# Optimization experiments

Measured on AMD Instinct MI355X. Metric: run time of the kernel, lower is better.

The kernel has to match this reference:

```python
import jax, jax.numpy as jnp
import numpy as np

N, E, F_IN, HID, OUT, H = 50000, 500000, 128, 64, 64, 2
P_DROP = 0.2


def setup_inputs() -> dict:
    key = jax.random.key(0)
    ks = jax.random.split(key, 24)
    g = lambda k, shp: jax.random.normal(k, shp, jnp.float32) * 0.05
    inp = {
        "feat": jax.random.normal(ks[0], (N, F_IN), jnp.float32),
        "edge_src": jax.random.randint(ks[1], (E,), 0, N, jnp.int32),
        "edge_dst": jax.random.randint(ks[2], (E,), 0, N, jnp.int32),
        # feature-mask linears
        "Wmt": g(ks[3], (F_IN, F_IN)), "bmt": g(ks[4], (F_IN,)),
        "Wms": g(ks[5], (F_IN, F_IN)), "bms": g(ks[6], (F_IN,)),
        # SAGEConv layers (mean aggregator): self + neigh linear + bias
        "W1_self": g(ks[7], (F_IN, HID)), "W1_neigh": g(ks[8], (F_IN, HID)), "b1": g(ks[9], (HID,)),
        "W2_self": g(ks[10], (HID, OUT)), "W2_neigh": g(ks[11], (HID, OUT)), "b2": g(ks[12], (OUT,)),
        # GATv2Conv layers: fc_src, fc_dst, attn vector per head, bias
        "g1_Wsrc": g(ks[13], (F_IN, H * HID)), "g1_Wdst": g(ks[14], (F_IN, H * HID)),
        "g1_attn": g(ks[15], (H, HID)), "g1_bias": g(ks[16], (H * HID,)),
        "g2_Wsrc": g(ks[17], (HID, H * OUT)), "g2_Wdst": g(ks[18], (HID, H * OUT)),
        "g2_attn": g(ks[19], (H, OUT)), "g2_bias": g(ks[20], (H * OUT,)),
        # final projection
        "W3": g(ks[21], (OUT + F_IN, OUT)), "b3": g(ks[22], (OUT,)),
    }
    # deterministic (inverted) dropout masks, training=True, p=0.2
    keep = 1.0 - P_DROP
    km1, km2 = jax.random.split(ks[23])
    inp["drop_t"] = jax.random.bernoulli(km1, keep, (N, HID)).astype(jnp.float32) / keep
    inp["drop_s"] = jax.random.bernoulli(km2, keep, (N, HID)).astype(jnp.float32) / keep
    return inp


def _sage_mean(h, src, dst, W_self, W_neigh, b):
    # mean over in-neighbors, then linear (mean and linear commute)
    agg = jax.ops.segment_sum(h[src], dst, num_segments=N)          # [N,D]
    deg = jax.ops.segment_sum(jnp.ones((E,), h.dtype), dst, num_segments=N)
    h_neigh = agg / jnp.maximum(deg, 1.0)[:, None]
    return h @ W_self + h_neigh @ W_neigh + b


def _gatv2(h, src, dst, Wsrc, Wdst, attn, bias, heads, dout):
    fs = (h @ Wsrc).reshape(N, heads, dout)
    fd = (h @ Wdst).reshape(N, heads, dout)
    e = jax.nn.leaky_relu(fs[src] + fd[dst], 0.2)                   # [E,H,D]
    logits = jnp.einsum('ehd,hd->eh', e, attn)                      # [E,H]
    m = jax.ops.segment_max(logits, dst, num_segments=N)            # edge softmax per dst
    ex = jnp.exp(logits - m[dst])
    denom = jax.ops.segment_sum(ex, dst, num_segments=N)
    alpha = ex / denom[dst]                                         # [E,H]
    out = jax.ops.segment_sum(alpha[:, :, None] * fs[src], dst, num_segments=N)
    return out + bias.reshape(heads, dout)                          # [N,H,D]


def _l2norm(x):
    return x / jnp.maximum(jnp.linalg.norm(x, axis=1, keepdims=True), 1e-12)


def reference(feat, edge_src, edge_dst, Wmt, bmt, Wms, bms,
              W1_self, W1_neigh, b1, W2_self, W2_neigh, b2,
              g1_Wsrc, g1_Wdst, g1_attn, g1_bias,
              g2_Wsrc, g2_Wdst, g2_attn, g2_bias,
              W3, b3, drop_t, drop_s):
    gelu = lambda x: jax.nn.gelu(x, approximate=False)  # torch F.gelu default = exact erf
    # topology branch (SAGE)
    h_t = feat * jax.nn.sigmoid(feat @ Wmt + bmt)
    h_t = gelu(_sage_mean(h_t, edge_src, edge_dst, W1_self, W1_neigh, b1)) * drop_t
    h_t = gelu(_sage_mean(h_t, edge_src, edge_dst, W2_self, W2_neigh, b2))
    h_t = jnp.concatenate([h_t, feat], axis=1) @ W3 + b3
    h_t = _l2norm(jax.nn.leaky_relu(h_t, 0.01))
    # semantic branch (GATv2)
    h_s = feat * jax.nn.sigmoid(feat @ Wms + bms)
    h_s = gelu(_gatv2(h_s, edge_src, edge_dst, g1_Wsrc, g1_Wdst, g1_attn, g1_bias, H, HID)).mean(axis=1) * drop_s
    h_s = gelu(_gatv2(h_s, edge_src, edge_dst, g2_Wsrc, g2_Wdst, g2_attn, g2_bias, H, OUT)).mean(axis=1)
    h_s = _l2norm(h_s)
    return (h_t, h_s)
```

## Files before the change

### kernel.cpp

```cpp
#include <hip/hip_runtime.h>
#include <math.h>

constexpr int N_  = 50000;
constexpr int E_  = 500000;
constexpr int NB_ = (N_ + 255) / 256;

typedef unsigned short u16;
typedef unsigned int u32;
typedef short short8 __attribute__((ext_vector_type(8)));
typedef __bf16 bf16x8 __attribute__((ext_vector_type(8)));
typedef float f32x4 __attribute__((ext_vector_type(4)));
typedef short short4v __attribute__((ext_vector_type(4)));

#define DINL __device__ __forceinline__

DINL float gelu_f(float x) { return 0.5f * x * (1.f + erff(x * 0.70710678118654752f)); }
DINL float sigmoid_f(float x) { return 1.f / (1.f + expf(-x)); }
DINL u16 f2b(float x) {
  unsigned u = __float_as_uint(x);
  return (u16)((u + 0x7FFFu + ((u >> 16) & 1u)) >> 16);
}
DINL float b2f(u16 b) { return __uint_as_float(((unsigned)b) << 16); }

template <int CTRL>
DINL float dpp_add(float c) {
  int p = __builtin_amdgcn_update_dpp(0, __builtin_bit_cast(int, c), CTRL, 0xf, 0xf, false);
  return c + __builtin_bit_cast(float, p);
}
DINL float half_reduce(float c) {
  c = dpp_add<0xB1>(c);
  c = dpp_add<0x4E>(c);
  c = dpp_add<0x141>(c);
  c = dpp_add<0x140>(c);
  int p = __builtin_amdgcn_ds_swizzle(__builtin_bit_cast(int, c), 0x401F);
  return c + __builtin_bit_cast(float, p);
}

__global__ void deg_int_kernel(const int* __restrict__ dst, int* __restrict__ deg) {
  int t = blockIdx.x * 256 + threadIdx.x;
  if (t < E_) atomicAdd(&deg[dst[t]], 1);
}

__global__ __launch_bounds__(256) void scan_local(const int* __restrict__ deg,
    int* __restrict__ rowptr, int* __restrict__ bsum) {
  __shared__ int sums[4];
  const int tid = threadIdx.x, lane = tid & 63, wid = tid >> 6;
  const int i = blockIdx.x * 256 + tid;
  int v = (i < N_) ? deg[i] : 0;
  int x = v;
#pragma unroll
  for (int o = 1; o < 64; o <<= 1) { int y = __shfl_up(x, o); if (lane >= o) x += y; }
  if (lane == 63) sums[wid] = x;
  __syncthreads();
  int woff = 0;
#pragma unroll
  for (int w = 0; w < 3; ++w) if (w < wid) woff += sums[w];
  if (i < N_) rowptr[i] = x - v + woff;
  if (tid == 255) bsum[blockIdx.x] = woff + x;
}

__global__ __launch_bounds__(256) void scan_block(const int* __restrict__ bsum,
                                                  int* __restrict__ bpre) {
  __shared__ int sums[4];
  const int tid = threadIdx.x, lane = tid & 63, wid = tid >> 6;
  int v = (tid < NB_) ? bsum[tid] : 0;
  int x = v;
#pragma unroll
  for (int o = 1; o < 64; o <<= 1) { int y = __shfl_up(x, o); if (lane >= o) x += y; }
  if (lane == 63) sums[wid] = x;
  __syncthreads();
  int woff = 0;
#pragma unroll
  for (int w = 0; w < 3; ++w) if (w < wid) woff += sums[w];
  if (tid < NB_) bpre[tid] = x - v + woff;
  if (tid == 255) bpre[NB_] = woff + x;
}

__global__ __launch_bounds__(256) void scan_add(int* __restrict__ rowptr,
                                                const int* __restrict__ bpre) {
  int i = blockIdx.x * 256 + threadIdx.x;
  if (i < N_) rowptr[i] += bpre[i >> 8];
  else if (i == N_) rowptr[N_] = bpre[NB_];
}

__global__ void csr_fill(const int* __restrict__ src, const int* __restrict__ dst,
                         const int* __restrict__ rowptr, int* __restrict__ cursor,
                         int* __restrict__ colsrc) {
  int e = blockIdx.x * 256 + threadIdx.x;
  if (e >= E_) return;
  int d = dst[e];
  int pos = rowptr[d] + atomicAdd(&cursor[d], 1);
  colsrc[pos] = src[e];
}

__global__ __launch_bounds__(256) void pack_feat(const float* __restrict__ f,
                                                 u16* __restrict__ o) {
  int t = blockIdx.x * 256 + threadIdx.x;
  float4 v = ((const float4*)f)[t];
  short4v r;
  r[0] = (short)f2b(v.x); r[1] = (short)f2b(v.y);
  r[2] = (short)f2b(v.z); r[3] = (short)f2b(v.w);
  ((short4v*)o)[t] = r;
}

__global__ __launch_bounds__(256) void pack_w(
    const float* __restrict__ Wmt, const float* __restrict__ Wms,
    const float* __restrict__ W1s, const float* __restrict__ W1n,
    const float* __restrict__ W2s, const float* __restrict__ W2n,
    const float* __restrict__ g1Ws, const float* __restrict__ g1Wd,
    const float* __restrict__ g2Ws, const float* __restrict__ g2Wd,
    const float* __restrict__ W3, u16* __restrict__ dst) {
  int e = blockIdx.x * 256 + threadIdx.x;
  const float *Wa, *Wb = nullptr;
  int K1, K2 = 0, Ca, Cb = 0, st;
  if (e < 16384)       { Wa = Wmt;  K1 = 128; Ca = 128;           st = 0; }
  else if (e < 32768)  { Wa = Wms;  K1 = 128; Ca = 128;           st = 16384; }
  else if (e < 49152)  { Wa = W1s;  Wb = W1n; K1 = 128; K2 = 128; Ca = 64;  st = 32768; }
  else if (e < 57344)  { Wa = W2s;  Wb = W2n; K1 = 64;  K2 = 64;  Ca = 64;  st = 49152; }
  else if (e < 90112)  { Wa = g1Ws; Wb = g1Wd; K1 = 128; Ca = 128; Cb = 128; st = 57344; }
  else if (e < 106496) { Wa = g2Ws; Wb = g2Wd; K1 = 64;  Ca = 128; Cb = 128; st = 90112; }
  else                 { Wa = W3;   K1 = 192; Ca = 64;            st = 106496; }
  int el = e - st;
  int Kt = K1 + K2;
  int ct = el / (Kt * 16);
  int rem = el - ct * Kt * 16;
  int ks = rem >> 9, rem2 = rem & 511, lane = rem2 >> 3, j = rem2 & 7;
  int k = ks * 32 + ((lane >> 4) << 3) + j;
  int c = ct * 16 + (lane & 15);
  float v;
  if (k < K1) v = (c < Ca) ? Wa[k * Ca + c] : Wb[k * Cb + (c - Ca)];
  else        v = Wb[(k - K1) * Ca + c];
  dst[e] = f2b(v);
}

template <int K1, int K2, int C, int EPI>
__global__ __launch_bounds__(256) void gemm_mfma(
    const u16* __restrict__ A1, const u16* __restrict__ A2,
    const u16* __restrict__ Wp, const float* __restrict__ bias,
    const float* __restrict__ bias2, const float* __restrict__ mulf,
    void* __restrict__ outv, void* __restrict__ outv2) {
  constexpr int K = K1 + K2, KS = K / 32, CT4 = C / 64;
  constexpr int NCH1 = K1 / 8, NCH2 = K2 / 8;
  __shared__ u16 alds[64 * K];
  const int tid = threadIdx.x;
  const int w = tid >> 6, l = tid & 63;
  const int wr0 = blockIdx.x * 64;

  short8 wfrag[KS][CT4];
#pragma unroll
  for (int ks = 0; ks < KS; ++ks)
#pragma unroll
    for (int c4 = 0; c4 < CT4; ++c4)
      wfrag[ks][c4] = *(const short8*)(Wp +
          ((size_t)((w * CT4 + c4) * KS + ks) * 64 + l) * 8);

  for (int i = tid; i < 64 * NCH1; i += 256) {
    int rr = i / NCH1, kc = i % NCH1;
    int gr = wr0 + rr; if (gr >= N_) gr = N_ - 1;
    short8 v = *(const short8*)(A1 + (long)gr * K1 + kc * 8);
    *(short8*)&alds[rr * K + ((kc ^ (rr & 7)) << 3)] = v;
  }
  if constexpr (K2 > 0) {
    for (int i = tid; i < 64 * NCH2; i += 256) {
      int rr = i / NCH2, kc = i % NCH2;
      int gr = wr0 + rr; if (gr >= N_) gr = N_ - 1;
      short8 v = *(const short8*)(A2 + (long)gr * K2 + kc * 8);
      *(short8*)&alds[rr * K + (((NCH1 + kc) ^ (rr & 7)) << 3)] = v;
    }
  }
  __syncthreads();

  f32x4 acc[4][CT4];
#pragma unroll
  for (int rg = 0; rg < 4; ++rg)
#pragma unroll
    for (int c4 = 0; c4 < CT4; ++c4) acc[rg][c4] = (f32x4){0.f, 0.f, 0.f, 0.f};

#pragma unroll
  for (int ks = 0; ks < KS; ++ks) {
#pragma unroll
    for (int rg = 0; rg < 4; ++rg) {
      const int nr = rg * 16 + (l & 15);
      const int ch = (ks * 4 + (l >> 4)) ^ (nr & 7);
      short8 av = *(const short8*)&alds[nr * K + (ch << 3)];
      bf16x8 bf = __builtin_bit_cast(bf16x8, av);
#pragma unroll
      for (int c4 = 0; c4 < CT4; ++c4)
        acc[rg][c4] = __builtin_amdgcn_mfma_f32_16x16x32_bf16(
            __builtin_bit_cast(bf16x8, wfrag[ks][c4]), bf, acc[rg][c4], 0, 0, 0);
    }
  }

  const int colq = (l >> 4) << 2;
  if constexpr (EPI == 0) {
    u16* out = (u16*)outv;
#pragma unroll
    for (int rg = 0; rg < 4; ++rg) {
      int row = wr0 + rg * 16 + (l & 15);
      if (row >= N_) continue;
#pragma unroll
      for (int c4 = 0; c4 < CT4; ++c4) {
        int colb = (w * CT4 + c4) * 16 + colq;
        short4v s;
#pragma unroll
        for (int r = 0; r < 4; ++r) s[r] = (short)f2b(acc[rg][c4][r]);
        *(short4v*)(out + (long)row * C + colb) = s;
      }
    }
  } else if constexpr (EPI == 2 || EPI == 3) {
    u16* out = (u16*)outv;
    const int colb = w * 16 + colq;
    float4 bv = *(const float4*)(bias + colb);
#pragma unroll
    for (int rg = 0; rg < 4; ++rg) {
      int row = wr0 + rg * 16 + (l & 15);
      if (row >= N_) continue;
      float4 dv;
      if constexpr (EPI == 2) dv = *(const float4*)(mulf + (long)row * C + colb);
      short4v s;
#pragma unroll
      for (int r = 0; r < 4; ++r) {
        float g = gelu_f(acc[rg][0][r] + ((const float*)&bv)[r]);
        if constexpr (EPI == 2) g *= ((const float*)&dv)[r];
        s[r] = (short)f2b(g);
      }
      *(short4v*)(out + (long)row * C + colb) = s;
    }
  } else if constexpr (EPI == 4) {
    __shared__ float ssb[64][4];
    float* out = (float*)outv;
    const int colb = w * 16 + colq;
    float4 bv = *(const float4*)(bias + colb);
    float xv[4][4];
#pragma unroll
    for (int rg = 0; rg < 4; ++rg) {
      float ss = 0.f;
#pragma unroll
      for (int r = 0; r < 4; ++r) {
        float x = acc[rg][0][r] + ((const float*)&bv)[r];
        x = fmaxf(x, 0.01f * x);
        xv[rg][r] = x; ss += x * x;
      }
      ss += __shfl_xor(ss, 16);
      ss += __shfl_xor(ss, 32);
      if (l < 16) ssb[rg * 16 + l][w] = ss;
    }
    __syncthreads();
#pragma unroll
    for (int rg = 0; rg < 4; ++rg) {
      int nl = rg * 16 + (l & 15);
      int row = wr0 + nl;
      if (row >= N_) continue;
      float ss = ssb[nl][0] + ssb[nl][1] + ssb[nl][2] + ssb[nl][3];
      float sc = 1.f / fmaxf(sqrtf(ss), 1e-12f);
      float4 o;
#pragma unroll
      for (int r = 0; r < 4; ++r) ((float*)&o)[r] = xv[rg][r] * sc;
      *(float4*)(out + (long)row * 64 + colb) = o;
    }
  } else {
#pragma unroll
    for (int c4 = 0; c4 < CT4; ++c4) {
      const int ct = w * CT4 + c4;
      const bool lo = ct < 8;
      u16* op = lo ? (u16*)outv : (u16*)outv2;
      const int ccb = (ct & 7) * 16 + colq;
      float4 bv = *(const float4*)((lo ? bias : bias2) + ccb);
#pragma unroll
      for (int rg = 0; rg < 4; ++rg) {
        int nl = rg * 16 + (l & 15);
        int row = wr0 + nl;
        if (row >= N_) continue;
        int ch = (ccb >> 3) ^ (nl & 7);
        short4v fq = *(const short4v*)&alds[nl * K + (ch << 3) + (ccb & 7)];
        short4v s;
#pragma unroll
        for (int r = 0; r < 4; ++r) {
          float x = acc[rg][c4][r] + ((const float*)&bv)[r];
          float fv = b2f((u16)fq[r]);
          s[r] = (short)f2b(fv * sigmoid_f(x));
        }
        *(short4v*)(op + (long)row * 128 + ccb) = s;
      }
    }
  }
}

__global__ __launch_bounds__(256) void gather_bf128(const u16* __restrict__ h,
    const int* __restrict__ rowptr, const int* __restrict__ colsrc,
    u16* __restrict__ out) {
  int node = blockIdx.x * 4 + (threadIdx.x >> 6);
  int lane = threadIdx.x & 63;
  if (node >= N_) return;
  int beg = rowptr[node], end = rowptr[node + 1];
  float inv = 1.f / fmaxf((float)(end - beg), 1.f);
  float a0 = 0.f, a1 = 0.f, b0 = 0.f, b1 = 0.f;
  int j = beg;
  for (; j + 4 <= end; j += 4) {
    int s0 = colsrc[j], s1 = colsrc[j + 1], s2 = colsrc[j + 2], s3 = colsrc[j + 3];
    u32 v0 = *(const u32*)(h + (long)s0 * 128 + 2 * lane);
    u32 v1 = *(const u32*)(h + (long)s1 * 128 + 2 * lane);
    u32 v2 = *(const u32*)(h + (long)s2 * 128 + 2 * lane);
    u32 v3 = *(const u32*)(h + (long)s3 * 128 + 2 * lane);
    a0 += b2f((u16)(v0 & 0xffffu)) + b2f((u16)(v2 & 0xffffu));
    a1 += b2f((u16)(v0 >> 16))     + b2f((u16)(v2 >> 16));
    b0 += b2f((u16)(v1 & 0xffffu)) + b2f((u16)(v3 & 0xffffu));
    b1 += b2f((u16)(v1 >> 16))     + b2f((u16)(v3 >> 16));
  }
  for (; j < end; ++j) {
    int s = colsrc[j];
    u32 v = *(const u32*)(h + (long)s * 128 + 2 * lane);
    a0 += b2f((u16)(v & 0xffffu));
    a1 += b2f((u16)(v >> 16));
  }
  a0 += b0; a1 += b1;
  u32 r = (u32)f2b(a0 * inv) | ((u32)f2b(a1 * inv) << 16);
  *(u32*)(out + (long)node * 128 + 2 * lane) = r;
}

__global__ __launch_bounds__(256) void gather_bf64(const u16* __restrict__ h,
    const int* __restrict__ rowptr, const int* __restrict__ colsrc,
    u16* __restrict__ out) {
  int node = blockIdx.x * 4 + (threadIdx.x >> 6);
  int lane = threadIdx.x & 63;
  if (node >= N_) return;
  int beg = rowptr[node], end = rowptr[node + 1];
  int half = lane >> 5, cl = lane & 31;
  float a0 = 0.f, a1 = 0.f, b0 = 0.f, b1 = 0.f;
  int j = beg;
  for (; j + 4 <= end; j += 4) {
    int s0 = colsrc[j + half], s1 = colsrc[j + 2 + half];
    u32 v0 = *(const u32*)(h + (long)s0 * 64 + 2 * cl);
    u32 v1 = *(const u32*)(h + (long)s1 * 64 + 2 * cl);
    a0 += b2f((u16)(v0 & 0xffffu));
    a1 += b2f((u16)(v0 >> 16));
    b0 += b2f((u16)(v1 & 0xffffu));
    b1 += b2f((u16)(v1 >> 16));
  }
  for (; j + half < end; j += 2) {
    int s = colsrc[j + half];
    u32 v = *(const u32*)(h + (long)s * 64 + 2 * cl);
    a0 += b2f((u16)(v & 0xffffu));
    a1 += b2f((u16)(v >> 16));
  }
  a0 += b0; a1 += b1;
  a0 += __shfl_xor(a0, 32);
  a1 += __shfl_xor(a1, 32);
  if (lane < 32) {
    float inv = 1.f / fmaxf((float)(end - beg), 1.f);
    u32 r = (u32)f2b(a0 * inv) | ((u32)f2b(a1 * inv) << 16);
    *(u32*)(out + (long)node * 64 + 2 * lane) = r;
  }
}

template <bool LAYER1>
__global__ __launch_bounds__(256) void gat_fused(const u16* __restrict__ fsfd,
    const int* __restrict__ rowptr, const int* __restrict__ colsrc,
    const float* __restrict__ attn, const float* __restrict__ bias,
    const float* __restrict__ drop, void* __restrict__ outv) {
  int node = blockIdx.x * 4 + (threadIdx.x >> 6);
  int lane = threadIdx.x & 63;
  if (node >= N_) return;
  float2 av = *(const float2*)(attn + 2 * lane);
  u32 fdv = *(const u32*)(fsfd + (long)node * 256 + 128 + 2 * lane);
  float fd0 = b2f((u16)(fdv & 0xffffu)), fd1 = b2f((u16)(fdv >> 16));
  float d_own = 0.f, acc0 = 0.f, acc1 = 0.f;
  const int beg = rowptr[node], end = rowptr[node + 1];
  int j = beg;
  for (; j + 4 <= end; j += 4) {
    int s0 = colsrc[j], s1 = colsrc[j + 1], s2 = colsrc[j + 2], s3 = colsrc[j + 3];
    u32 v0 = *(const u32*)(fsfd + (long)s0 * 256 + 2 * lane);
    u32 v1 = *(const u32*)(fsfd + (long)s1 * 256 + 2 * lane);
    u32 v2 = *(const u32*)(fsfd + (long)s2 * 256 + 2 * lane);
    u32 v3 = *(const u32*)(fsfd + (long)s3 * 256 + 2 * lane);
    float f00 = b2f((u16)(v0 & 0xffffu)), f01 = b2f((u16)(v0 >> 16));
    float f10 = b2f((u16)(v1 & 0xffffu)), f11 = b2f((u16)(v1 >> 16));
    float f20 = b2f((u16)(v2 & 0xffffu)), f21 = b2f((u16)(v2 >> 16));
    float f30 = b2f((u16)(v3 & 0xffffu)), f31 = b2f((u16)(v3 >> 16));
    float x00 = f00 + fd0; x00 = fmaxf(x00, 0.2f * x00);
    float x01 = f01 + fd1; x01 = fmaxf(x01, 0.2f * x01);
    float x10 = f10 + fd0; x10 = fmaxf(x10, 0.2f * x10);
    float x11 = f11 + fd1; x11 = fmaxf(x11, 0.2f * x11);
    float x20 = f20 + fd0; x20 = fmaxf(x20, 0.2f * x20);
    float x21 = f21 + fd1; x21 = fmaxf(x21, 0.2f * x21);
    float x30 = f30 + fd0; x30 = fmaxf(x30, 0.2f * x30);
    float x31 = f31 + fd1; x31 = fmaxf(x31, 0.2f * x31);
    float c0 = half_reduce(x00 * av.x + x01 * av.y);
    float c1 = half_reduce(x10 * av.x + x11 * av.y);
    float c2 = half_reduce(x20 * av.x + x21 * av.y);
    float c3 = half_reduce(x30 * av.x + x31 * av.y);
    float e0 = __expf(c0), e1 = __expf(c1), e2 = __expf(c2), e3 = __expf(c3);
    d_own += (e0 + e1) + (e2 + e3);
    acc0 += e0 * f00 + e1 * f10 + e2 * f20 + e3 * f30;
    acc1 += e0 * f01 + e1 * f11 + e2 * f21 + e3 * f31;
  }
  for (; j < end; ++j) {
    int s = colsrc[j];
    u32 fv = *(const u32*)(fsfd + (long)s * 256 + 2 * lane);
    float f0 = b2f((u16)(fv & 0xffffu)), f1 = b2f((u16)(fv >> 16));
    float x0 = f0 + fd0; x0 = fmaxf(x0, 0.2f * x0);
    float x1 = f1 + fd1; x1 = fmaxf(x1, 0.2f * x1);
    float c = half_reduce(x0 * av.x + x1 * av.y);
    float e = __expf(c);
    d_own += e;
    acc0 += e * f0;
    acc1 += e * f1;
  }
  float2 bv = *(const float2*)(bias + 2 * lane);
  float inv = d_own > 0.f ? 1.f / d_own : 0.f;
  float g0 = gelu_f(bv.x + acc0 * inv);
  float g1 = gelu_f(bv.y + acc1 * inv);
  float v0 = 0.5f * (g0 + __shfl_xor(g0, 32));
  float v1 = 0.5f * (g1 + __shfl_xor(g1, 32));
  if constexpr (LAYER1) {
    if (lane < 32) {
      float2 dv = *(const float2*)(drop + (long)node * 64 + 2 * lane);
      u32 r = (u32)f2b(v0 * dv.x) | ((u32)f2b(v1 * dv.y) << 16);
      *(u32*)((u16*)outv + (long)node * 64 + 2 * lane) = r;
    }
  } else {
    float ss = v0 * v0 + v1 * v1;
#pragma unroll
    for (int o = 16; o; o >>= 1) ss += __shfl_xor(ss, o);
    float sc = 1.f / fmaxf(sqrtf(ss), 1e-12f);
    if (lane < 32) {
      float2 r; r.x = v0 * sc; r.y = v1 * sc;
      *(float2*)((float*)outv + (long)node * 64 + 2 * lane) = r;
    }
  }
}

extern "C" void kernel_launch(void* const* d_in, const int* in_sizes, int n_in,
                              void* d_out, int out_size, void* d_ws, size_t ws_size,
                              hipStream_t stream) {
  const float* feat = (const float*)d_in[0];
  const int*   esrc = (const int*)d_in[1];
  const int*   edst = (const int*)d_in[2];
  const float* Wmt = (const float*)d_in[3],  *bmt = (const float*)d_in[4];
  const float* Wms = (const float*)d_in[5],  *bms = (const float*)d_in[6];
  const float* W1s = (const float*)d_in[7],  *W1n = (const float*)d_in[8],  *b1 = (const float*)d_in[9];
  const float* W2s = (const float*)d_in[10], *W2n = (const float*)d_in[11], *b2 = (const float*)d_in[12];
  const float* g1Ws = (const float*)d_in[13], *g1Wd = (const float*)d_in[14];
  const float* g1a  = (const float*)d_in[15], *g1b  = (const float*)d_in[16];
  const float* g2Ws = (const float*)d_in[17], *g2Wd = (const float*)d_in[18];
  const float* g2a  = (const float*)d_in[19], *g2b  = (const float*)d_in[20];
  const float* W3  = (const float*)d_in[21], *b3 = (const float*)d_in[22];
  const float* dropt = (const float*)d_in[23], *drops = (const float*)d_in[24];

  float* out_t = (float*)d_out;
  float* out_s = out_t + (long)N_ * 64;

  u16* wsh = (u16*)d_ws;
  u16* featbf = wsh;
  u16* hbuf_t = wsh +  6400000;
  u16* hbuf_s = wsh + 12800000;
  u16* hn     = wsh + 19200000;
  u16* h1     = wsh + 25600000;
  u16* hn2    = wsh + 28800000;
  u16* h2     = wsh + 32000000;
  u16* hs1    = wsh + 35200000;
  u16* fsfd   = wsh + 38400000;
  u16* Wpk    = wsh + 51200000;
  int* degi   = (int*)(wsh + 51318784);
  int* cursor = degi + N_;
  int* rowptr = cursor + N_;
  int* colsrc = rowptr + N_ + 1;
  int* bsum   = colsrc + E_;
  int* bpre   = bsum + NB_;

  const u16* WpMT = Wpk;
  const u16* WpS1 = Wpk + 32768;
  const u16* WpS2 = Wpk + 49152;
  const u16* WpG1 = Wpk + 57344;
  const u16* WpG2 = Wpk + 90112;
  const u16* WpW3 = Wpk + 106496;

  constexpr int GB = (N_ + 63) / 64;

  (void)hipMemsetAsync(degi, 0, (size_t)(2 * N_) * sizeof(int), stream);
  deg_int_kernel<<<(E_ + 255) / 256, 256, 0, stream>>>(edst, degi);
  scan_local<<<NB_, 256, 0, stream>>>(degi, rowptr, bsum);
  scan_block<<<1, 256, 0, stream>>>(bsum, bpre);
  scan_add<<<(N_ + 256) / 256, 256, 0, stream>>>(rowptr, bpre);
  csr_fill<<<(E_ + 255) / 256, 256, 0, stream>>>(esrc, edst, rowptr, cursor, colsrc);
  pack_feat<<<N_ * 128 / 4 / 256, 256, 0, stream>>>(feat, featbf);
  pack_w<<<464, 256, 0, stream>>>(Wmt, Wms, W1s, W1n, W2s, W2n,
                                  g1Ws, g1Wd, g2Ws, g2Wd, W3, Wpk);

  gemm_mfma<128, 0, 256, 5><<<GB, 256, 0, stream>>>(featbf, nullptr, WpMT, bmt, bms,
                                                    nullptr, hbuf_t, hbuf_s);

  gather_bf128<<<N_ / 4, 256, 0, stream>>>(hbuf_t, rowptr, colsrc, hn);
  gemm_mfma<128, 128, 64, 2><<<GB, 256, 0, stream>>>(hbuf_t, hn, WpS1, b1, nullptr,
                                                     dropt, h1, nullptr);
  gather_bf64<<<N_ / 4, 256, 0, stream>>>(h1, rowptr, colsrc, hn2);
  gemm_mfma<64, 64, 64, 3><<<GB, 256, 0, stream>>>(h1, hn2, WpS2, b2, nullptr,
                                                   nullptr, h2, nullptr);
  gemm_mfma<64, 128, 64, 4><<<GB, 256, 0, stream>>>(h2, featbf, WpW3, b3, nullptr,
                                                    nullptr, out_t, nullptr);

  gemm_mfma<128, 0, 256, 0><<<GB, 256, 0, stream>>>(hbuf_s, nullptr, WpG1, nullptr, nullptr,
                                                    nullptr, fsfd, nullptr);
  gat_fused<true><<<N_ / 4, 256, 0, stream>>>(fsfd, rowptr, colsrc, g1a, g1b, drops, hs1);
  gemm_mfma<64, 0, 256, 0><<<GB, 256, 0, stream>>>(hs1, nullptr, WpG2, nullptr, nullptr,
                                                   nullptr, fsfd, nullptr);
  gat_fused<false><<<N_ / 4, 256, 0, stream>>>(fsfd, rowptr, colsrc, g2a, g2b, nullptr, out_s);
}
```

Before: 280.0 us.

## Process multiple edges per wave with 8-byte loads in gather and GAT kernels

The gather and GATv2 aggregation kernels now give each lane 4 features through 8-byte loads. Each wave therefore splits into halves or quarters that handle different edges at once, and the partial sums are combined with cross-lane shuffles at the end. The per-edge attention reduction shrinks from 32 lanes to 16, which removes the ds_swizzle step. Tails are handled with masked lanes. The `node >= N_` guard was removed, which is safe only if the grid exactly covers N (50000/4 divides evenly).

```diff
diff --git a/kernel.cpp b/kernel.cpp
--- a/kernel.cpp
+++ b/kernel.cpp
@@ -27,13 +27,12 @@
   int p = __builtin_amdgcn_update_dpp(0, __builtin_bit_cast(int, c), CTRL, 0xf, 0xf, false);
   return c + __builtin_bit_cast(float, p);
 }
-DINL float half_reduce(float c) {
+DINL float reduce16(float c) {
   c = dpp_add<0xB1>(c);
   c = dpp_add<0x4E>(c);
   c = dpp_add<0x141>(c);
   c = dpp_add<0x140>(c);
-  int p = __builtin_amdgcn_ds_swizzle(__builtin_bit_cast(int, c), 0x401F);
-  return c + __builtin_bit_cast(float, p);
+  return c;
 }
 
 __global__ void deg_int_kernel(const int* __restrict__ dst, int* __restrict__ deg) {
@@ -290,66 +289,98 @@
     const int* __restrict__ rowptr, const int* __restrict__ colsrc,
     u16* __restrict__ out) {
   int node = blockIdx.x * 4 + (threadIdx.x >> 6);
-  int lane = threadIdx.x & 63;
-  if (node >= N_) return;
+  int l = threadIdx.x & 63;
+  int hl = l & 31, half = l >> 5;
   int beg = rowptr[node], end = rowptr[node + 1];
   float inv = 1.f / fmaxf((float)(end - beg), 1.f);
-  float a0 = 0.f, a1 = 0.f, b0 = 0.f, b1 = 0.f;
+  float a0 = 0.f, a1 = 0.f, a2 = 0.f, a3 = 0.f;
+  float b0 = 0.f, b1 = 0.f, b2 = 0.f, b3 = 0.f;
+  const int off = 4 * hl;
   int j = beg;
-  for (; j + 4 <= end; j += 4) {
-    int s0 = colsrc[j], s1 = colsrc[j + 1], s2 = colsrc[j + 2], s3 = colsrc[j + 3];
-    u32 v0 = *(const u32*)(h + (long)s0 * 128 + 2 * lane);
-    u32 v1 = *(const u32*)(h + (long)s1 * 128 + 2 * lane);
-    u32 v2 = *(const u32*)(h + (long)s2 * 128 + 2 * lane);
-    u32 v3 = *(const u32*)(h + (long)s3 * 128 + 2 * lane);
-    a0 += b2f((u16)(v0 & 0xffffu)) + b2f((u16)(v2 & 0xffffu));
-    a1 += b2f((u16)(v0 >> 16))     + b2f((u16)(v2 >> 16));
-    b0 += b2f((u16)(v1 & 0xffffu)) + b2f((u16)(v3 & 0xffffu));
-    b1 += b2f((u16)(v1 >> 16))     + b2f((u16)(v3 >> 16));
-  }
-  for (; j < end; ++j) {
-    int s = colsrc[j];
-    u32 v = *(const u32*)(h + (long)s * 128 + 2 * lane);
-    a0 += b2f((u16)(v & 0xffffu));
-    a1 += b2f((u16)(v >> 16));
-  }
-  a0 += b0; a1 += b1;
-  u32 r = (u32)f2b(a0 * inv) | ((u32)f2b(a1 * inv) << 16);
-  *(u32*)(out + (long)node * 128 + 2 * lane) = r;
+  for (; j + 8 <= end; j += 8) {
+    int sa = colsrc[j + half],     sb = colsrc[j + 2 + half];
+    int sc = colsrc[j + 4 + half], sd = colsrc[j + 6 + half];
+    uint2 va = *(const uint2*)(h + (size_t)sa * 128 + off);
+    uint2 vb = *(const uint2*)(h + (size_t)sb * 128 + off);
+    uint2 vc = *(const uint2*)(h + (size_t)sc * 128 + off);
+    uint2 vd = *(const uint2*)(h + (size_t)sd * 128 + off);
+    a0 += b2f((u16)(va.x & 0xffffu)) + b2f((u16)(vc.x & 0xffffu));
+    a1 += b2f((u16)(va.x >> 16))     + b2f((u16)(vc.x >> 16));
+    a2 += b2f((u16)(va.y & 0xffffu)) + b2f((u16)(vc.y & 0xffffu));
+    a3 += b2f((u16)(va.y >> 16))     + b2f((u16)(vc.y >> 16));
+    b0 += b2f((u16)(vb.x & 0xffffu)) + b2f((u16)(vd.x & 0xffffu));
+    b1 += b2f((u16)(vb.x >> 16))     + b2f((u16)(vd.x >> 16));
+    b2 += b2f((u16)(vb.y & 0xffffu)) + b2f((u16)(vd.y & 0xffffu));
+    b3 += b2f((u16)(vb.y >> 16))     + b2f((u16)(vd.y >> 16));
+  }
+  for (; j < end; j += 2) {
+    int idx = j + half;
+    bool valid = idx < end;
+    int s = colsrc[valid ? idx : end - 1];
+    uint2 v = *(const uint2*)(h + (size_t)s * 128 + off);
+    if (!valid) { v.x = 0; v.y = 0; }
+    a0 += b2f((u16)(v.x & 0xffffu));
+    a1 += b2f((u16)(v.x >> 16));
+    a2 += b2f((u16)(v.y & 0xffffu));
+    a3 += b2f((u16)(v.y >> 16));
+  }
+  a0 += b0; a1 += b1; a2 += b2; a3 += b3;
+  a0 += __shfl_xor(a0, 32); a1 += __shfl_xor(a1, 32);
+  a2 += __shfl_xor(a2, 32); a3 += __shfl_xor(a3, 32);
+  if (l < 32) {
+    short4v s;
+    s[0] = (short)f2b(a0 * inv); s[1] = (short)f2b(a1 * inv);
+    s[2] = (short)f2b(a2 * inv); s[3] = (short)f2b(a3 * inv);
+    *(short4v*)(out + (long)node * 128 + off) = s;
+  }
 }
 
 __global__ __launch_bounds__(256) void gather_bf64(const u16* __restrict__ h,
     const int* __restrict__ rowptr, const int* __restrict__ colsrc,
     u16* __restrict__ out) {
   int node = blockIdx.x * 4 + (threadIdx.x >> 6);
-  int lane = threadIdx.x & 63;
-  if (node >= N_) return;
+  int l = threadIdx.x & 63;
+  int ql = l & 15, qg = l >> 4;
   int beg = rowptr[node], end = rowptr[node + 1];
-  int half = lane >> 5, cl = lane & 31;
-  float a0 = 0.f, a1 = 0.f, b0 = 0.f, b1 = 0.f;
+  float a0 = 0.f, a1 = 0.f, a2 = 0.f, a3 = 0.f;
+  float b0 = 0.f, b1 = 0.f, b2 = 0.f, b3 = 0.f;
+  const int off = 4 * ql;
   int j = beg;
-  for (; j + 4 <= end; j += 4) {
-    int s0 = colsrc[j + half], s1 = colsrc[j + 2 + half];
-    u32 v0 = *(const u32*)(h + (long)s0 * 64 + 2 * cl);
-    u32 v1 = *(const u32*)(h + (long)s1 * 64 + 2 * cl);
-    a0 += b2f((u16)(v0 & 0xffffu));
-    a1 += b2f((u16)(v0 >> 16));
-    b0 += b2f((u16)(v1 & 0xffffu));
-    b1 += b2f((u16)(v1 >> 16));
-  }
-  for (; j + half < end; j += 2) {
-    int s = colsrc[j + half];
-    u32 v = *(const u32*)(h + (long)s * 64 + 2 * cl);
-    a0 += b2f((u16)(v & 0xffffu));
-    a1 += b2f((u16)(v >> 16));
-  }
-  a0 += b0; a1 += b1;
-  a0 += __shfl_xor(a0, 32);
-  a1 += __shfl_xor(a1, 32);
-  if (lane < 32) {
+  for (; j + 8 <= end; j += 8) {
+    int s0 = colsrc[j + qg], s1 = colsrc[j + 4 + qg];
+    uint2 v0 = *(const uint2*)(h + (size_t)s0 * 64 + off);
+    uint2 v1 = *(const uint2*)(h + (size_t)s1 * 64 + off);
+    a0 += b2f((u16)(v0.x & 0xffffu));
+    a1 += b2f((u16)(v0.x >> 16));
+    a2 += b2f((u16)(v0.y & 0xffffu));
+    a3 += b2f((u16)(v0.y >> 16));
+    b0 += b2f((u16)(v1.x & 0xffffu));
+    b1 += b2f((u16)(v1.x >> 16));
+    b2 += b2f((u16)(v1.y & 0xffffu));
+    b3 += b2f((u16)(v1.y >> 16));
+  }
+  for (; j < end; j += 4) {
+    int idx = j + qg;
+    bool valid = idx < end;
+    int s = colsrc[valid ? idx : end - 1];
+    uint2 v = *(const uint2*)(h + (size_t)s * 64 + off);
+    if (!valid) { v.x = 0; v.y = 0; }
+    a0 += b2f((u16)(v.x & 0xffffu));
+    a1 += b2f((u16)(v.x >> 16));
+    a2 += b2f((u16)(v.y & 0xffffu));
+    a3 += b2f((u16)(v.y >> 16));
+  }
+  a0 += b0; a1 += b1; a2 += b2; a3 += b3;
+  a0 += __shfl_xor(a0, 32); a1 += __shfl_xor(a1, 32);
+  a2 += __shfl_xor(a2, 32); a3 += __shfl_xor(a3, 32);
+  a0 += __shfl_xor(a0, 16); a1 += __shfl_xor(a1, 16);
+  a2 += __shfl_xor(a2, 16); a3 += __shfl_xor(a3, 16);
+  if (l < 16) {
     float inv = 1.f / fmaxf((float)(end - beg), 1.f);
-    u32 r = (u32)f2b(a0 * inv) | ((u32)f2b(a1 * inv) << 16);
-    *(u32*)(out + (long)node * 64 + 2 * lane) = r;
+    short4v s;
+    s[0] = (short)f2b(a0 * inv); s[1] = (short)f2b(a1 * inv);
+    s[2] = (short)f2b(a2 * inv); s[3] = (short)f2b(a3 * inv);
+    *(short4v*)(out + (long)node * 64 + off) = s;
   }
 }
 
@@ -359,73 +390,77 @@
     const float* __restrict__ attn, const float* __restrict__ bias,
     const float* __restrict__ drop, void* __restrict__ outv) {
   int node = blockIdx.x * 4 + (threadIdx.x >> 6);
-  int lane = threadIdx.x & 63;
-  if (node >= N_) return;
-  float2 av = *(const float2*)(attn + 2 * lane);
-  u32 fdv = *(const u32*)(fsfd + (long)node * 256 + 128 + 2 * lane);
-  float fd0 = b2f((u16)(fdv & 0xffffu)), fd1 = b2f((u16)(fdv >> 16));
-  float d_own = 0.f, acc0 = 0.f, acc1 = 0.f;
+  int l = threadIdx.x & 63;
+  int hl = l & 31, half = l >> 5;
+  const int off = 4 * hl;
+  float4 av = *(const float4*)(attn + off);
+  uint2 fdv = *(const uint2*)(fsfd + (size_t)node * 256 + 128 + off);
+  float fd0 = b2f((u16)(fdv.x & 0xffffu)), fd1 = b2f((u16)(fdv.x >> 16));
+  float fd2 = b2f((u16)(fdv.y & 0xffffu)), fd3 = b2f((u16)(fdv.y >> 16));
+  float d_own = 0.f, acc0 = 0.f, acc1 = 0.f, acc2 = 0.f, acc3 = 0.f;
+
+  auto edge = [&](uint2 v, float m) {
+    float f0 = b2f((u16)(v.x & 0xffffu)), f1 = b2f((u16)(v.x >> 16));
+    float f2 = b2f((u16)(v.y & 0xffffu)), f3 = b2f((u16)(v.y >> 16));
+    float t0 = f0 + fd0, t1 = f1 + fd1, t2 = f2 + fd2, t3 = f3 + fd3;
+    t0 = fmaxf(t0, 0.2f * t0); t1 = fmaxf(t1, 0.2f * t1);
+    t2 = fmaxf(t2, 0.2f * t2); t3 = fmaxf(t3, 0.2f * t3);
+    float c = t0 * av.x + t1 * av.y + t2 * av.z + t3 * av.w;
+    c = reduce16(c);
+    float e = __expf(c) * m;
+    d_own += e;
+    acc0 += e * f0; acc1 += e * f1; acc2 += e * f2; acc3 += e * f3;
+  };
+
   const int beg = rowptr[node], end = rowptr[node + 1];
   int j = beg;
-  for (; j + 4 <= end; j += 4) {
-    int s0 = colsrc[j], s1 = colsrc[j + 1], s2 = colsrc[j + 2], s3 = colsrc[j + 3];
-    u32 v0 = *(const u32*)(fsfd + (long)s0 * 256 + 2 * lane);
-    u32 v1 = *(const u32*)(fsfd + (long)s1 * 256 + 2 * lane);
-    u32 v2 = *(const u32*)(fsfd + (long)s2 * 256 + 2 * lane);
-    u32 v3 = *(const u32*)(fsfd + (long)s3 * 256 + 2 * lane);
-    float f00 = b2f((u16)(v0 & 0xffffu)), f01 = b2f((u16)(v0 >> 16));
-    float f10 = b2f((u16)(v1 & 0xffffu)), f11 = b2f((u16)(v1 >> 16));
-    float f20 = b2f((u16)(v2 & 0xffffu)), f21 = b2f((u16)(v2 >> 16));
-    float f30 = b2f((u16)(v3 & 0xffffu)), f31 = b2f((u16)(v3 >> 16));
-    float x00 = f00 + fd0; x00 = fmaxf(x00, 0.2f * x00);
-    float x01 = f01 + fd1; x01 = fmaxf(x01, 0.2f * x01);
-    float x10 = f10 + fd0; x10 = fmaxf(x10, 0.2f * x10);
-    float x11 = f11 + fd1; x11 = fmaxf(x11, 0.2f * x11);
-    float x20 = f20 + fd0; x20 = fmaxf(x20, 0.2f * x20);
-    float x21 = f21 + fd1; x21 = fmaxf(x21, 0.2f * x21);
-    float x30 = f30 + fd0; x30 = fmaxf(x30, 0.2f * x30);
-    float x31 = f31 + fd1; x31 = fmaxf(x31, 0.2f * x31);
-    float c0 = half_reduce(x00 * av.x + x01 * av.y);
-    float c1 = half_reduce(x10 * av.x + x11 * av.y);
-    float c2 = half_reduce(x20 * av.x + x21 * av.y);
-    float c3 = half_reduce(x30 * av.x + x31 * av.y);
-    float e0 = __expf(c0), e1 = __expf(c1), e2 = __expf(c2), e3 = __expf(c3);
-    d_own += (e0 + e1) + (e2 + e3);
-    acc0 += e0 * f00 + e1 * f10 + e2 * f20 + e3 * f30;
-    acc1 += e0 * f01 + e1 * f11 + e2 * f21 + e3 * f31;
-  }
-  for (; j < end; ++j) {
-    int s = colsrc[j];
-    u32 fv = *(const u32*)(fsfd + (long)s * 256 + 2 * lane);
-    float f0 = b2f((u16)(fv & 0xffffu)), f1 = b2f((u16)(fv >> 16));
-    float x0 = f0 + fd0; x0 = fmaxf(x0, 0.2f * x0);
-    float x1 = f1 + fd1; x1 = fmaxf(x1, 0.2f * x1);
-    float c = half_reduce(x0 * av.x + x1 * av.y);
-    float e = __expf(c);
-    d_own += e;
-    acc0 += e * f0;
-    acc1 += e * f1;
-  }
-  float2 bv = *(const float2*)(bias + 2 * lane);
+  for (; j + 8 <= end; j += 8) {
+    int sa = colsrc[j + half],     sb = colsrc[j + 2 + half];
+    int sc = colsrc[j + 4 + half], sd = colsrc[j + 6 + half];
+    uint2 va = *(const uint2*)(fsfd + (size_t)sa * 256 + off);
+    uint2 vb = *(const uint2*)(fsfd + (size_t)sb * 256 + off);
+    uint2 vc = *(const uint2*)(fsfd + (size_t)sc * 256 + off);
+    uint2 vd = *(const uint2*)(fsfd + (size_t)sd * 256 + off);
+    edge(va, 1.f); edge(vb, 1.f); edge(vc, 1.f); edge(vd, 1.f);
+  }
+  for (; j < end; j += 2) {
+    int idx = j + half;
+    bool valid = idx < end;
+    int s = colsrc[valid ? idx : end - 1];
+    uint2 v = *(const uint2*)(fsfd + (size_t)s * 256 + off);
+    if (!valid) { v.x = 0; v.y = 0; }
+    edge(v, valid ? 1.f : 0.f);
+  }
+
+  acc0 += __shfl_xor(acc0, 32); acc1 += __shfl_xor(acc1, 32);
+  acc2 += __shfl_xor(acc2, 32); acc3 += __shfl_xor(acc3, 32);
+  d_own += __shfl_xor(d_own, 32);
+
+  float4 bv = *(const float4*)(bias + off);
   float inv = d_own > 0.f ? 1.f / d_own : 0.f;
   float g0 = gelu_f(bv.x + acc0 * inv);
   float g1 = gelu_f(bv.y + acc1 * inv);
-  float v0 = 0.5f * (g0 + __shfl_xor(g0, 32));
-  float v1 = 0.5f * (g1 + __shfl_xor(g1, 32));
+  float g2 = gelu_f(bv.z + acc2 * inv);
+  float g3 = gelu_f(bv.w + acc3 * inv);
+  float v0 = 0.5f * (g0 + __shfl_xor(g0, 16));
+  float v1 = 0.5f * (g1 + __shfl_xor(g1, 16));
+  float v2 = 0.5f * (g2 + __shfl_xor(g2, 16));
+  float v3 = 0.5f * (g3 + __shfl_xor(g3, 16));
   if constexpr (LAYER1) {
-    if (lane < 32) {
-      float2 dv = *(const float2*)(drop + (long)node * 64 + 2 * lane);
-      u32 r = (u32)f2b(v0 * dv.x) | ((u32)f2b(v1 * dv.y) << 16);
-      *(u32*)((u16*)outv + (long)node * 64 + 2 * lane) = r;
+    if (l < 16) {
+      float4 dv = *(const float4*)(drop + (long)node * 64 + 4 * l);
+      short4v s;
+      s[0] = (short)f2b(v0 * dv.x); s[1] = (short)f2b(v1 * dv.y);
+      s[2] = (short)f2b(v2 * dv.z); s[3] = (short)f2b(v3 * dv.w);
+      *(short4v*)((u16*)outv + (long)node * 64 + 4 * l) = s;
     }
   } else {
-    float ss = v0 * v0 + v1 * v1;
-#pragma unroll
-    for (int o = 16; o; o >>= 1) ss += __shfl_xor(ss, o);
+    float ss = v0 * v0 + v1 * v1 + v2 * v2 + v3 * v3;
+    ss = reduce16(ss);
     float sc = 1.f / fmaxf(sqrtf(ss), 1e-12f);
-    if (lane < 32) {
-      float2 r; r.x = v0 * sc; r.y = v1 * sc;
-      *(float2*)((float*)outv + (long)node * 64 + 2 * lane) = r;
+    if (l < 16) {
+      float4 o; o.x = v0 * sc; o.y = v1 * sc; o.z = v2 * sc; o.w = v3 * sc;
+      *(float4*)((float*)outv + (long)node * 64 + 4 * l) = o;
     }
   }
 }
```

Result: no change. 274.6 us (-1.9%).
